# Performance work log

Measured on AMD Instinct MI355X. Metric: run time of the kernel, lower is better.

The kernel has to match this reference:

```python
import jax, jax.numpy as jnp
import numpy as np

N_MODES, BATCH, PH, PW = 4, 1024, 128, 128
OBJ_C, OBJ_H, OBJ_W = 1, 2048, 2048


def setup_inputs() -> dict:
    key = jax.random.key(0)
    k1, k2, k3 = jax.random.split(key, 3)
    obj = jax.random.normal(k1, (OBJ_C, OBJ_H, OBJ_W), dtype=jnp.float32)
    waves = jax.random.normal(k2, (N_MODES, BATCH, PH, PW), dtype=jnp.float32)
    pos = jax.random.randint(k3, (BATCH, 2), 0, OBJ_H - PH, dtype=jnp.int32)
    return {"obj": obj, "waves": waves, "pos": pos}


def reference(obj, waves, pos):
    B, H, W = waves.shape[1], waves.shape[2], waves.shape[3]
    # patch_norm = sum over probe modes of |waves|^2  -> [B, H, W]
    patch_norm = jnp.sum(waves * waves, axis=0)
    # overlap_intensity: scatter-add each patch into object_norm at its corner pos
    rows = pos[:, 0, None] + jnp.arange(H)          # [B, H]
    cols = pos[:, 1, None] + jnp.arange(W)          # [B, W]
    object_norm = jnp.zeros(obj.shape[1:], jnp.float32).at[
        rows[:, :, None], cols[:, None, :]
    ].add(patch_norm)
    # batch_crop: gather object patches at each position -> [B, C, H, W]
    C = obj.shape[0]
    def crop_one(p):
        return jax.lax.dynamic_slice(obj, (0, p[0], p[1]), (C, H, W))
    patches = jax.vmap(crop_one)(pos)
    return patches, object_norm
```

## Files before the change

### kernel.cpp

```cpp
#include <hip/hip_runtime.h>


#define NMODES 4
#define NB     1024
#define PH     128
#define PW     128
#define OH     2048
#define OW     2048

#define TS       64
#define NT_X     (OW / TS)
#define NT_Y     (OH / TS)
#define NT       (NT_X * NT_Y)
#define CAP      128
#define SLICES   8
#define UNROLL   4

__global__ __launch_bounds__(256) void crop_and_bin(
    const float* __restrict__ obj,
    const int*   __restrict__ pos,
    float* __restrict__ patches,
    int*   __restrict__ tile_cnt,
    int*   __restrict__ tile_list)
{
    const int q = blockIdx.x * blockDim.x + threadIdx.x;

    if (q < NB) {
        const int r0 = pos[2 * q];
        const int c0 = pos[2 * q + 1];
        const int ty0 = r0 >> 6, ty1 = (r0 + PH - 1) >> 6;
        const int tx0 = c0 >> 6, tx1 = (c0 + PW - 1) >> 6;
        for (int ty = ty0; ty <= ty1; ++ty)
            for (int tx = tx0; tx <= tx1; ++tx) {
                const int t = ty * NT_X + tx;
                const int idx = atomicAdd(&tile_cnt[t], 1);
                if (idx < CAP) tile_list[t * CAP + idx] = q;
            }
    }

    const int b     = q >> 12;
    const int local = q & 4095;
    const int h     = local >> 5;
    const int w     = (local & 31) << 2;

    const int r0 = pos[b * 2 + 0];
    const int c0 = pos[b * 2 + 1];

    const int oidx = (r0 + h) * OW + (c0 + w);
    float4 p;
    p.x = obj[oidx + 0];
    p.y = obj[oidx + 1];
    p.z = obj[oidx + 2];
    p.w = obj[oidx + 3];
    *reinterpret_cast<float4*>(patches + b * (PH * PW) + h * PW + w) = p;
}

__global__ __launch_bounds__(256) void norm_gather(
    const float* __restrict__ waves,
    const int*   __restrict__ pos,
    const int*   __restrict__ tile_cnt,
    const int*   __restrict__ tile_list,
    float* __restrict__ norm)
{
    const int blk = blockIdx.x;
    const int t   = blk >> 3;
    const int s   = blk & 7;
    const int Y0  = (t >> 5) * TS + s * (TS / SLICES);
    const int X0  = (t & 31) * TS;

    __shared__ int s_base[CAP + UNROLL];
    __shared__ int s_r[CAP + UNROLL];
    __shared__ int s_c[CAP + UNROLL];

    const int count = min(tile_cnt[t], CAP);
    const int cpad  = (count + UNROLL - 1) & ~(UNROLL - 1);
    for (int i = threadIdx.x; i < cpad; i += 256) {
        if (i < count) {
            const int b = tile_list[t * CAP + i];
            s_base[i] = b * (PH * PW);
            s_r[i]    = pos[2 * b];
            s_c[i]    = pos[2 * b + 1];
        } else {
            s_base[i] = 0;
            s_r[i]    = 1 << 20;
            s_c[i]    = 1 << 20;
        }
    }
    __syncthreads();

    const int x     = threadIdx.x & 63;
    const int phase = threadIdx.x >> 6;
    const int X     = X0 + x;
    const int Ya    = Y0 + phase;
    const int Yb    = Ya + 4;

    const int MS = NB * PH * PW;

    float acc_a = 0.0f;
    float acc_b = 0.0f;

    #pragma unroll UNROLL
    for (int i = 0; i < cpad; ++i) {
        const int dra = Ya - s_r[i];
        const int drb = Yb - s_r[i];
        const int dc  = X  - s_c[i];

        const bool va = ((unsigned)dc < (unsigned)PW) &
                        ((unsigned)dra < (unsigned)PH);
        const bool vb = ((unsigned)dc < (unsigned)PW) &
                        ((unsigned)drb < (unsigned)PH);

        const int dcc  = min(max(dc, 0),  PW - 1);
        const int drac = min(max(dra, 0), PH - 1);
        const int drbc = min(max(drb, 0), PH - 1);

        const float* wa = waves + s_base[i] + drac * PW + dcc;
        const float* wb = waves + s_base[i] + drbc * PW + dcc;

        const float a0 = wa[0];
        const float a1 = wa[MS];
        const float a2 = wa[2 * MS];
        const float a3 = wa[3 * MS];
        const float b0 = wb[0];
        const float b1 = wb[MS];
        const float b2 = wb[2 * MS];
        const float b3 = wb[3 * MS];

        const float sa = a0 * a0 + a1 * a1 + a2 * a2 + a3 * a3;
        const float sb = b0 * b0 + b1 * b1 + b2 * b2 + b3 * b3;
        acc_a += va ? sa : 0.0f;
        acc_b += vb ? sb : 0.0f;
    }

    norm[Ya * OW + X] = acc_a;
    norm[Yb * OW + X] = acc_b;
}

extern "C" void kernel_launch(void* const* d_in, const int* in_sizes, int n_in,
                              void* d_out, int out_size, void* d_ws, size_t ws_size,
                              hipStream_t stream) {
    const float* obj   = (const float*)d_in[0];
    const float* waves = (const float*)d_in[1];
    const int*   pos   = (const int*)d_in[2];

    float* patches = (float*)d_out;
    float* norm    = (float*)d_out + (size_t)NB * PH * PW;

    int* tile_cnt  = (int*)d_ws;
    int* tile_list = tile_cnt + NT;

    hipMemsetAsync(tile_cnt, 0, NT * sizeof(int), stream);

    const int quads = NB * PH * PW / 4;
    crop_and_bin<<<quads / 256, 256, 0, stream>>>(obj, pos, patches,
                                                  tile_cnt, tile_list);
    norm_gather<<<NT * SLICES, 256, 0, stream>>>(waves, pos, tile_cnt,
                                                 tile_list, norm);
}
```

Before: 411.8 us.

## Precompute per-patch mode-summed norm in crop kernel before tile gather

The crop kernel now also streams the four wave modes with coalesced float4 loads and writes a per-patch sum of squares into a workspace buffer. The gather kernel then reads one value per overlapping patch instead of four scattered loads per mode. This trades an extra 64 MB write and re-read for far fewer uncoalesced gathers across overlapping patches. The old path is kept as a fallback when the workspace is too small.

After: 431.0 us. +4.7%, slower.

```diff
diff --git a/kernel.cpp b/kernel.cpp
--- a/kernel.cpp
+++ b/kernel.cpp
@@ -16,10 +16,12 @@
 #define SLICES   8
 #define UNROLL   4
 
-__global__ __launch_bounds__(256) void crop_and_bin(
+__global__ __launch_bounds__(256) void crop_reduce_bin(
     const float* __restrict__ obj,
+    const float* __restrict__ waves,
     const int*   __restrict__ pos,
     float* __restrict__ patches,
+    float* __restrict__ pnorm,
     int*   __restrict__ tile_cnt,
     int*   __restrict__ tile_list)
 {
@@ -52,11 +54,24 @@
     p.y = obj[oidx + 1];
     p.z = obj[oidx + 2];
     p.w = obj[oidx + 3];
-    *reinterpret_cast<float4*>(patches + b * (PH * PW) + h * PW + w) = p;
-}
-
-__global__ __launch_bounds__(256) void norm_gather(
-    const float* __restrict__ waves,
+    const int pbase = b * (PH * PW) + h * PW + w;
+    *reinterpret_cast<float4*>(patches + pbase) = p;
+
+    const int MS = NB * PH * PW;
+    const float4 w0 = *reinterpret_cast<const float4*>(waves + pbase);
+    const float4 w1 = *reinterpret_cast<const float4*>(waves + MS + pbase);
+    const float4 w2 = *reinterpret_cast<const float4*>(waves + 2 * MS + pbase);
+    const float4 w3 = *reinterpret_cast<const float4*>(waves + 3 * MS + pbase);
+    float4 s;
+    s.x = w0.x * w0.x + w1.x * w1.x + w2.x * w2.x + w3.x * w3.x;
+    s.y = w0.y * w0.y + w1.y * w1.y + w2.y * w2.y + w3.y * w3.y;
+    s.z = w0.z * w0.z + w1.z * w1.z + w2.z * w2.z + w3.z * w3.z;
+    s.w = w0.w * w0.w + w1.w * w1.w + w2.w * w2.w + w3.w * w3.w;
+    *reinterpret_cast<float4*>(pnorm + pbase) = s;
+}
+
+__global__ __launch_bounds__(256) void norm_gather_pn(
+    const float* __restrict__ pnorm,
     const int*   __restrict__ pos,
     const int*   __restrict__ tile_cnt,
     const int*   __restrict__ tile_list,
@@ -94,12 +109,119 @@
     const int Ya    = Y0 + phase;
     const int Yb    = Ya + 4;
 
-    const int MS = NB * PH * PW;
-
     float acc_a = 0.0f;
     float acc_b = 0.0f;
 
-    #pragma unroll UNROLL
+    #pragma unroll 4
+    for (int i = 0; i < cpad; ++i) {
+        const int dra = Ya - s_r[i];
+        const int drb = Yb - s_r[i];
+        const int dc  = X  - s_c[i];
+
+        const bool va = ((unsigned)dc < (unsigned)PW) &
+                        ((unsigned)dra < (unsigned)PH);
+        const bool vb = ((unsigned)dc < (unsigned)PW) &
+                        ((unsigned)drb < (unsigned)PH);
+
+        const int dcc  = min(max(dc, 0),  PW - 1);
+        const int drac = min(max(dra, 0), PH - 1);
+        const int drbc = min(max(drb, 0), PH - 1);
+
+        const float sa = pnorm[s_base[i] + drac * PW + dcc];
+        const float sb = pnorm[s_base[i] + drbc * PW + dcc];
+
+        acc_a += va ? sa : 0.0f;
+        acc_b += vb ? sb : 0.0f;
+    }
+
+    norm[Ya * OW + X] = acc_a;
+    norm[Yb * OW + X] = acc_b;
+}
+
+__global__ __launch_bounds__(256) void crop_and_bin(
+    const float* __restrict__ obj,
+    const int*   __restrict__ pos,
+    float* __restrict__ patches,
+    int*   __restrict__ tile_cnt,
+    int*   __restrict__ tile_list)
+{
+    const int q = blockIdx.x * blockDim.x + threadIdx.x;
+
+    if (q < NB) {
+        const int r0 = pos[2 * q];
+        const int c0 = pos[2 * q + 1];
+        const int ty0 = r0 >> 6, ty1 = (r0 + PH - 1) >> 6;
+        const int tx0 = c0 >> 6, tx1 = (c0 + PW - 1) >> 6;
+        for (int ty = ty0; ty <= ty1; ++ty)
+            for (int tx = tx0; tx <= tx1; ++tx) {
+                const int t = ty * NT_X + tx;
+                const int idx = atomicAdd(&tile_cnt[t], 1);
+                if (idx < CAP) tile_list[t * CAP + idx] = q;
+            }
+    }
+
+    const int b     = q >> 12;
+    const int local = q & 4095;
+    const int h     = local >> 5;
+    const int w     = (local & 31) << 2;
+
+    const int r0 = pos[b * 2 + 0];
+    const int c0 = pos[b * 2 + 1];
+
+    const int oidx = (r0 + h) * OW + (c0 + w);
+    float4 p;
+    p.x = obj[oidx + 0];
+    p.y = obj[oidx + 1];
+    p.z = obj[oidx + 2];
+    p.w = obj[oidx + 3];
+    *reinterpret_cast<float4*>(patches + b * (PH * PW) + h * PW + w) = p;
+}
+
+__global__ __launch_bounds__(256) void norm_gather_waves(
+    const float* __restrict__ waves,
+    const int*   __restrict__ pos,
+    const int*   __restrict__ tile_cnt,
+    const int*   __restrict__ tile_list,
+    float* __restrict__ norm)
+{
+    const int blk = blockIdx.x;
+    const int t   = blk >> 3;
+    const int s   = blk & 7;
+    const int Y0  = (t >> 5) * TS + s * (TS / SLICES);
+    const int X0  = (t & 31) * TS;
+
+    __shared__ int s_base[CAP + UNROLL];
+    __shared__ int s_r[CAP + UNROLL];
+    __shared__ int s_c[CAP + UNROLL];
+
+    const int count = min(tile_cnt[t], CAP);
+    const int cpad  = (count + UNROLL - 1) & ~(UNROLL - 1);
+    for (int i = threadIdx.x; i < cpad; i += 256) {
+        if (i < count) {
+            const int b = tile_list[t * CAP + i];
+            s_base[i] = b * (PH * PW);
+            s_r[i]    = pos[2 * b];
+            s_c[i]    = pos[2 * b + 1];
+        } else {
+            s_base[i] = 0;
+            s_r[i]    = 1 << 20;
+            s_c[i]    = 1 << 20;
+        }
+    }
+    __syncthreads();
+
+    const int x     = threadIdx.x & 63;
+    const int phase = threadIdx.x >> 6;
+    const int X     = X0 + x;
+    const int Ya    = Y0 + phase;
+    const int Yb    = Ya + 4;
+
+    const int MS = NB * PH * PW;
+
+    float acc_a = 0.0f;
+    float acc_b = 0.0f;
+
+    #pragma unroll 4
     for (int i = 0; i < cpad; ++i) {
         const int dra = Ya - s_r[i];
         const int drb = Yb - s_r[i];
@@ -146,14 +268,26 @@
     float* patches = (float*)d_out;
     float* norm    = (float*)d_out + (size_t)NB * PH * PW;
 
-    int* tile_cnt  = (int*)d_ws;
-    int* tile_list = tile_cnt + NT;
+    int*   tile_cnt  = (int*)d_ws;
+    int*   tile_list = tile_cnt + NT;
+    float* pnorm     = (float*)(tile_list + (size_t)NT * CAP);
+
+    const size_t ws_need = (size_t)(NT + (size_t)NT * CAP) * sizeof(int)
+                         + (size_t)NB * PH * PW * sizeof(float);
 
     hipMemsetAsync(tile_cnt, 0, NT * sizeof(int), stream);
 
     const int quads = NB * PH * PW / 4;
-    crop_and_bin<<<quads / 256, 256, 0, stream>>>(obj, pos, patches,
-                                                  tile_cnt, tile_list);
-    norm_gather<<<NT * SLICES, 256, 0, stream>>>(waves, pos, tile_cnt,
-                                                 tile_list, norm);
-}
+
+    if (ws_size >= ws_need) {
+        crop_reduce_bin<<<quads / 256, 256, 0, stream>>>(
+            obj, waves, pos, patches, pnorm, tile_cnt, tile_list);
+        norm_gather_pn<<<NT * SLICES, 256, 0, stream>>>(
+            pnorm, pos, tile_cnt, tile_list, norm);
+    } else {
+        crop_and_bin<<<quads / 256, 256, 0, stream>>>(
+            obj, pos, patches, tile_cnt, tile_list);
+        norm_gather_waves<<<NT * SLICES, 256, 0, stream>>>(
+            waves, pos, tile_cnt, tile_list, norm);
+    }
+}
```

## Shrink binning tiles to 32x32 and compute four rows per thread

Applied to the files above, without the earlier changes.

Object-space binning tiles go from 64x64 to 32x32, so each tile's candidate list is shorter and each output pixel tests fewer non-overlapping patches. Slicing is dropped: one block now covers a whole 32x32 tile, and each thread accumulates four rows, reusing the column test and shared-memory entry across them. Smaller tiles mean each patch is registered in more tiles during binning, which adds atomics. CAP is halved to 64, so dense tiles could overflow and silently drop contributions.

After: 430.1 us. 4.5% more time.

```diff
diff --git a/kernel.cpp b/kernel.cpp
--- a/kernel.cpp
+++ b/kernel.cpp
@@ -8,12 +8,11 @@
 #define OH     2048
 #define OW     2048
 
-#define TS       64
+#define TS       32
 #define NT_X     (OW / TS)
 #define NT_Y     (OH / TS)
 #define NT       (NT_X * NT_Y)
-#define CAP      128
-#define SLICES   8
+#define CAP      64
 #define UNROLL   4
 
 __global__ __launch_bounds__(256) void crop_and_bin(
@@ -28,8 +27,8 @@
     if (q < NB) {
         const int r0 = pos[2 * q];
         const int c0 = pos[2 * q + 1];
-        const int ty0 = r0 >> 6, ty1 = (r0 + PH - 1) >> 6;
-        const int tx0 = c0 >> 6, tx1 = (c0 + PW - 1) >> 6;
+        const int ty0 = r0 >> 5, ty1 = (r0 + PH - 1) >> 5;
+        const int tx0 = c0 >> 5, tx1 = (c0 + PW - 1) >> 5;
         for (int ty = ty0; ty <= ty1; ++ty)
             for (int tx = tx0; tx <= tx1; ++tx) {
                 const int t = ty * NT_X + tx;
@@ -62,11 +61,9 @@
     const int*   __restrict__ tile_list,
     float* __restrict__ norm)
 {
-    const int blk = blockIdx.x;
-    const int t   = blk >> 3;
-    const int s   = blk & 7;
-    const int Y0  = (t >> 5) * TS + s * (TS / SLICES);
-    const int X0  = (t & 31) * TS;
+    const int t  = blockIdx.x;
+    const int Y0 = (t >> 6) * TS;
+    const int X0 = (t & 63) * TS;
 
     __shared__ int s_base[CAP + UNROLL];
     __shared__ int s_r[CAP + UNROLL];
@@ -88,52 +85,65 @@
     }
     __syncthreads();
 
-    const int x     = threadIdx.x & 63;
-    const int phase = threadIdx.x >> 6;
+    const int x     = threadIdx.x & 31;
+    const int phase = threadIdx.x >> 5;
     const int X     = X0 + x;
-    const int Ya    = Y0 + phase;
-    const int Yb    = Ya + 4;
+    const int Y     = Y0 + phase;
 
     const int MS = NB * PH * PW;
 
-    float acc_a = 0.0f;
-    float acc_b = 0.0f;
+    float acc0 = 0.0f, acc1 = 0.0f, acc2 = 0.0f, acc3 = 0.0f;
 
-    #pragma unroll UNROLL
+    #pragma unroll 2
     for (int i = 0; i < cpad; ++i) {
-        const int dra = Ya - s_r[i];
-        const int drb = Yb - s_r[i];
-        const int dc  = X  - s_c[i];
+        const int r0 = s_r[i];
+        const int c0 = s_c[i];
+        const int bb = s_base[i];
 
-        const bool va = ((unsigned)dc < (unsigned)PW) &
-                        ((unsigned)dra < (unsigned)PH);
-        const bool vb = ((unsigned)dc < (unsigned)PW) &
-                        ((unsigned)drb < (unsigned)PH);
+        const int dc  = X - c0;
+        const bool vc = (unsigned)dc < (unsigned)PW;
+        const int dcc = min(max(dc, 0), PW - 1);
 
-        const int dcc  = min(max(dc, 0),  PW - 1);
-        const int drac = min(max(dra, 0), PH - 1);
-        const int drbc = min(max(drb, 0), PH - 1);
+        const int dr0 = Y      - r0;
+        const int dr1 = Y + 8  - r0;
+        const int dr2 = Y + 16 - r0;
+        const int dr3 = Y + 24 - r0;
 
-        const float* wa = waves + s_base[i] + drac * PW + dcc;
-        const float* wb = waves + s_base[i] + drbc * PW + dcc;
+        const bool v0 = vc & ((unsigned)dr0 < (unsigned)PH);
+        const bool v1 = vc & ((unsigned)dr1 < (unsigned)PH);
+        const bool v2 = vc & ((unsigned)dr2 < (unsigned)PH);
+        const bool v3 = vc & ((unsigned)dr3 < (unsigned)PH);
 
-        const float a0 = wa[0];
-        const float a1 = wa[MS];
-        const float a2 = wa[2 * MS];
-        const float a3 = wa[3 * MS];
-        const float b0 = wb[0];
-        const float b1 = wb[MS];
-        const float b2 = wb[2 * MS];
-        const float b3 = wb[3 * MS];
+        const int drc0 = min(max(dr0, 0), PH - 1);
+        const int drc1 = min(max(dr1, 0), PH - 1);
+        const int drc2 = min(max(dr2, 0), PH - 1);
+        const int drc3 = min(max(dr3, 0), PH - 1);
 
-        const float sa = a0 * a0 + a1 * a1 + a2 * a2 + a3 * a3;
-        const float sb = b0 * b0 + b1 * b1 + b2 * b2 + b3 * b3;
-        acc_a += va ? sa : 0.0f;
-        acc_b += vb ? sb : 0.0f;
+        const float* w0p = waves + bb + drc0 * PW + dcc;
+        const float* w1p = waves + bb + drc1 * PW + dcc;
+        const float* w2p = waves + bb + drc2 * PW + dcc;
+        const float* w3p = waves + bb + drc3 * PW + dcc;
+
+        const float a0 = w0p[0], a1 = w0p[MS], a2 = w0p[2 * MS], a3 = w0p[3 * MS];
+        const float b0 = w1p[0], b1 = w1p[MS], b2 = w1p[2 * MS], b3 = w1p[3 * MS];
+        const float c0f = w2p[0], c1 = w2p[MS], c2 = w2p[2 * MS], c3 = w2p[3 * MS];
+        const float d0 = w3p[0], d1 = w3p[MS], d2 = w3p[2 * MS], d3 = w3p[3 * MS];
+
+        const float s0 = a0 * a0 + a1 * a1 + a2 * a2 + a3 * a3;
+        const float s1 = b0 * b0 + b1 * b1 + b2 * b2 + b3 * b3;
+        const float s2 = c0f * c0f + c1 * c1 + c2 * c2 + c3 * c3;
+        const float s3 = d0 * d0 + d1 * d1 + d2 * d2 + d3 * d3;
+
+        acc0 += v0 ? s0 : 0.0f;
+        acc1 += v1 ? s1 : 0.0f;
+        acc2 += v2 ? s2 : 0.0f;
+        acc3 += v3 ? s3 : 0.0f;
     }
 
-    norm[Ya * OW + X] = acc_a;
-    norm[Yb * OW + X] = acc_b;
+    norm[(Y     ) * OW + X] = acc0;
+    norm[(Y +  8) * OW + X] = acc1;
+    norm[(Y + 16) * OW + X] = acc2;
+    norm[(Y + 24) * OW + X] = acc3;
 }
 
 extern "C" void kernel_launch(void* const* d_in, const int* in_sizes, int n_in,
@@ -154,6 +164,6 @@
     const int quads = NB * PH * PW / 4;
     crop_and_bin<<<quads / 256, 256, 0, stream>>>(obj, pos, patches,
                                                   tile_cnt, tile_list);
-    norm_gather<<<NT * SLICES, 256, 0, stream>>>(waves, pos, tile_cnt,
-                                                 tile_list, norm);
+    norm_gather<<<NT, 256, 0, stream>>>(waves, pos, tile_cnt,
+                                        tile_list, norm);
 }
```

## Replace tile-binned gather with fused crop and atomic scatter-add of wave norms

Applied to the files above, without the earlier changes.

Drops the tile binning pass and the gather kernel. One fused kernel now crops object patches and, for each patch quad, reads the four mode waves with vectorized nontemporal loads. It reduces them to |w|^2 and scatter-adds the result into the norm with float atomics. The norm buffer is zeroed with a memset. This removes the indirect per-tile loop, the CAP truncation and the divergent reads, but adds heavy global float atomic traffic wherever patches overlap, and makes the summation order nondeterministic.

Result: slower. 565.6 us (+37.3%).

```diff
diff --git a/kernel.cpp b/kernel.cpp
--- a/kernel.cpp
+++ b/kernel.cpp
@@ -8,36 +8,16 @@
 #define OH     2048
 #define OW     2048
 
-#define TS       64
-#define NT_X     (OW / TS)
-#define NT_Y     (OH / TS)
-#define NT       (NT_X * NT_Y)
-#define CAP      128
-#define SLICES   8
-#define UNROLL   4
+typedef float vfloat4 __attribute__((ext_vector_type(4)));
 
-__global__ __launch_bounds__(256) void crop_and_bin(
+__global__ __launch_bounds__(256) void crop_reduce_scatter(
     const float* __restrict__ obj,
+    const float* __restrict__ waves,
     const int*   __restrict__ pos,
     float* __restrict__ patches,
-    int*   __restrict__ tile_cnt,
-    int*   __restrict__ tile_list)
+    float* __restrict__ norm)
 {
-    const int q = blockIdx.x * blockDim.x + threadIdx.x;
-
-    if (q < NB) {
-        const int r0 = pos[2 * q];
-        const int c0 = pos[2 * q + 1];
-        const int ty0 = r0 >> 6, ty1 = (r0 + PH - 1) >> 6;
-        const int tx0 = c0 >> 6, tx1 = (c0 + PW - 1) >> 6;
-        for (int ty = ty0; ty <= ty1; ++ty)
-            for (int tx = tx0; tx <= tx1; ++tx) {
-                const int t = ty * NT_X + tx;
-                const int idx = atomicAdd(&tile_cnt[t], 1);
-                if (idx < CAP) tile_list[t * CAP + idx] = q;
-            }
-    }
-
+    const int q     = blockIdx.x * blockDim.x + threadIdx.x;
     const int b     = q >> 12;
     const int local = q & 4095;
     const int h     = local >> 5;
@@ -47,93 +27,30 @@
     const int c0 = pos[b * 2 + 1];
 
     const int oidx = (r0 + h) * OW + (c0 + w);
-    float4 p;
+    vfloat4 p;
     p.x = obj[oidx + 0];
     p.y = obj[oidx + 1];
     p.z = obj[oidx + 2];
     p.w = obj[oidx + 3];
-    *reinterpret_cast<float4*>(patches + b * (PH * PW) + h * PW + w) = p;
-}
-
-__global__ __launch_bounds__(256) void norm_gather(
-    const float* __restrict__ waves,
-    const int*   __restrict__ pos,
-    const int*   __restrict__ tile_cnt,
-    const int*   __restrict__ tile_list,
-    float* __restrict__ norm)
-{
-    const int blk = blockIdx.x;
-    const int t   = blk >> 3;
-    const int s   = blk & 7;
-    const int Y0  = (t >> 5) * TS + s * (TS / SLICES);
-    const int X0  = (t & 31) * TS;
-
-    __shared__ int s_base[CAP + UNROLL];
-    __shared__ int s_r[CAP + UNROLL];
-    __shared__ int s_c[CAP + UNROLL];
-
-    const int count = min(tile_cnt[t], CAP);
-    const int cpad  = (count + UNROLL - 1) & ~(UNROLL - 1);
-    for (int i = threadIdx.x; i < cpad; i += 256) {
-        if (i < count) {
-            const int b = tile_list[t * CAP + i];
-            s_base[i] = b * (PH * PW);
-            s_r[i]    = pos[2 * b];
-            s_c[i]    = pos[2 * b + 1];
-        } else {
-            s_base[i] = 0;
-            s_r[i]    = 1 << 20;
-            s_c[i]    = 1 << 20;
-        }
-    }
-    __syncthreads();
-
-    const int x     = threadIdx.x & 63;
-    const int phase = threadIdx.x >> 6;
-    const int X     = X0 + x;
-    const int Ya    = Y0 + phase;
-    const int Yb    = Ya + 4;
+    const int pbase = b * (PH * PW) + h * PW + w;
+    __builtin_nontemporal_store(p, reinterpret_cast<vfloat4*>(patches + pbase));
 
     const int MS = NB * PH * PW;
+    const vfloat4 w0 = __builtin_nontemporal_load(
+        reinterpret_cast<const vfloat4*>(waves + pbase));
+    const vfloat4 w1 = __builtin_nontemporal_load(
+        reinterpret_cast<const vfloat4*>(waves + MS + pbase));
+    const vfloat4 w2 = __builtin_nontemporal_load(
+        reinterpret_cast<const vfloat4*>(waves + 2 * MS + pbase));
+    const vfloat4 w3 = __builtin_nontemporal_load(
+        reinterpret_cast<const vfloat4*>(waves + 3 * MS + pbase));
 
-    float acc_a = 0.0f;
-    float acc_b = 0.0f;
+    const vfloat4 s = w0 * w0 + w1 * w1 + w2 * w2 + w3 * w3;
 
-    #pragma unroll UNROLL
-    for (int i = 0; i < cpad; ++i) {
-        const int dra = Ya - s_r[i];
-        const int drb = Yb - s_r[i];
-        const int dc  = X  - s_c[i];
-
-        const bool va = ((unsigned)dc < (unsigned)PW) &
-                        ((unsigned)dra < (unsigned)PH);
-        const bool vb = ((unsigned)dc < (unsigned)PW) &
-                        ((unsigned)drb < (unsigned)PH);
-
-        const int dcc  = min(max(dc, 0),  PW - 1);
-        const int drac = min(max(dra, 0), PH - 1);
-        const int drbc = min(max(drb, 0), PH - 1);
-
-        const float* wa = waves + s_base[i] + drac * PW + dcc;
-        const float* wb = waves + s_base[i] + drbc * PW + dcc;
-
-        const float a0 = wa[0];
-        const float a1 = wa[MS];
-        const float a2 = wa[2 * MS];
-        const float a3 = wa[3 * MS];
-        const float b0 = wb[0];
-        const float b1 = wb[MS];
-        const float b2 = wb[2 * MS];
-        const float b3 = wb[3 * MS];
-
-        const float sa = a0 * a0 + a1 * a1 + a2 * a2 + a3 * a3;
-        const float sb = b0 * b0 + b1 * b1 + b2 * b2 + b3 * b3;
-        acc_a += va ? sa : 0.0f;
-        acc_b += vb ? sb : 0.0f;
-    }
-
-    norm[Ya * OW + X] = acc_a;
-    norm[Yb * OW + X] = acc_b;
+    atomicAdd(&norm[oidx + 0], s.x);
+    atomicAdd(&norm[oidx + 1], s.y);
+    atomicAdd(&norm[oidx + 2], s.z);
+    atomicAdd(&norm[oidx + 3], s.w);
 }
 
 extern "C" void kernel_launch(void* const* d_in, const int* in_sizes, int n_in,
@@ -146,14 +63,9 @@
     float* patches = (float*)d_out;
     float* norm    = (float*)d_out + (size_t)NB * PH * PW;
 
-    int* tile_cnt  = (int*)d_ws;
-    int* tile_list = tile_cnt + NT;
-
-    hipMemsetAsync(tile_cnt, 0, NT * sizeof(int), stream);
+    (void)hipMemsetAsync(norm, 0, (size_t)OH * OW * sizeof(float), stream);
 
     const int quads = NB * PH * PW / 4;
-    crop_and_bin<<<quads / 256, 256, 0, stream>>>(obj, pos, patches,
-                                                  tile_cnt, tile_list);
-    norm_gather<<<NT * SLICES, 256, 0, stream>>>(waves, pos, tile_cnt,
-                                                 tile_list, norm);
+    crop_reduce_scatter<<<quads / 256, 256, 0, stream>>>(obj, waves, pos,
+                                                         patches, norm);
 }
```
